# Kernel optimization log

Measured on AMD Instinct MI355X. Metric: run time of the kernel, lower is better.

Reference implementation:

```python
import jax, jax.numpy as jnp
import numpy as np

LMAX = 4
S2_DIM = (LMAX + 1) ** 2                                  # 25: s2 irreps, mul 1 per l
SO3_DIM = sum((2 * l + 1) ** 2 for l in range(LMAX + 1))  # 165: so3 irreps, mul 2l+1 per l
B = 2048
F_S2, F_SO3 = 1, 16
N_S2_KERNEL = 48      # s2_healpix_grid(rec_level=1)
N_SO3_KERNEL = 192    # so3_near_identity_grid()
N_ACT_GRID = 4000     # SO3Activation resolution=10, aspect_ratio=2 -> 20x10x20, flattened
N_EVAL = 4608         # so3_healpix_grid(rec_level=2): 192 pixels x 24 gamma


def setup_inputs() -> dict:
    ks = jax.random.split(jax.random.key(0), 7)
    return {
        "x": jax.random.normal(ks[0], (B, F_S2, S2_DIM), jnp.float32),
        "w_s2": jax.random.normal(ks[1], (F_S2, F_SO3, N_S2_KERNEL), jnp.float32),
        "Y": jax.random.normal(ks[2], (N_S2_KERNEL, S2_DIM), jnp.float32),
        "w_so3": jax.random.normal(ks[3], (F_SO3, 1, N_SO3_KERNEL), jnp.float32),
        "D_kernel": jax.random.normal(ks[4], (N_SO3_KERNEL, SO3_DIM), jnp.float32),
        "D_act": jax.random.normal(ks[5], (N_ACT_GRID, SO3_DIM), jnp.float32),
        "eval_wigners": jax.random.normal(ks[6], (SO3_DIM, N_EVAL), jnp.float32) / np.sqrt(SO3_DIM),
    }


def _s2_to_so3_linear(x, psi):
    # e3nn o3.Linear(s2_irreps -> so3_irreps, f_in, f_out, external weights)
    # x:   [B, f_in, 25]  (mul 1 per degree l)
    # psi: [f_in, f_out, 25] ; column l^2+j is the weight to output-multiplicity j of degree l
    f_in, f_out = psi.shape[0], psi.shape[1]
    out, s = [], 0
    for l in range(LMAX + 1):
        d = 2 * l + 1
        x_l = x[..., s:s + d]                       # [B, f_in, d]
        p_l = psi[..., s:s + d]                     # [f_in, f_out, d] (j = out-mul idx)
        o = jnp.einsum('bxm,xyj->byjm', x_l, p_l) / np.sqrt(f_in)
        out.append(o.reshape(x.shape[0], f_out, d * d))
        s += d
    return jnp.concatenate(out, axis=-1)            # [B, f_out, 165]


def _so3_to_so3_linear(x, psi):
    # e3nn o3.Linear(so3_irreps -> so3_irreps, f_in, f_out, external weights)
    # x:   [B, f_in, 165] ; psi: [f_in, f_out, 165]
    f_in, f_out = psi.shape[0], psi.shape[1]
    out, s = [], 0
    for l in range(LMAX + 1):
        d = 2 * l + 1
        x_l = x[..., s:s + d * d].reshape(x.shape[0], f_in, d, d)   # [B,f_in,u,m]
        p_l = psi[..., s:s + d * d].reshape(f_in, f_out, d, d)      # [f_in,f_out,u,v]
        o = jnp.einsum('bxum,xyuv->byvm', x_l, p_l) / np.sqrt(f_in * d)
        out.append(o.reshape(x.shape[0], f_out, d * d))
        s += d * d
    return jnp.concatenate(out, axis=-1)            # [B, f_out, 165]


def _forward(x, w_s2, Y, w_so3, D_kernel, D_act, eval_wigners):
    # --- S2Convolution: kernel = SH-transform of grid weights, then irrep-wise linear
    psi1 = jnp.einsum('ni,xyn->xyi', Y, w_s2) / np.sqrt(N_S2_KERNEL)     # [1,16,25]
    h = _s2_to_so3_linear(x, psi1)                                        # [B,16,165]
    # --- SO3Activation: Fourier -> SO(3) grid -> relu -> Fourier
    g = jnp.einsum('bfi,gi->bfg', h, D_act) / np.sqrt(SO3_DIM)            # [B,16,4000]
    g = jax.nn.relu(g)
    h = jnp.einsum('bfg,gi->bfi', g, D_act) * (np.sqrt(SO3_DIM) / N_ACT_GRID)
    # --- SO3Convolution
    psi2 = jnp.einsum('ni,xyn->xyi', D_kernel, w_so3) / np.sqrt(N_SO3_KERNEL)  # [16,1,165]
    harmonics = _so3_to_so3_linear(h, psi2)                               # [B,1,165]
    # --- compute_probabilities: matmul with eval Wigner-D basis + softmax over grid
    probs = jax.nn.softmax(jnp.einsum('bfi,ie->be', harmonics, eval_wigners), axis=1)  # [B,4608]
    # --- top-k masking: zero out everything below the 5th-highest prob of sample 0
    fifth = jax.lax.top_k(probs, 5)[0][0, 4]
    probs = jnp.where(probs < fifth, 0.0, probs)
    return harmonics, probs


def reference(x, w_s2, Y, w_so3, D_kernel, D_act, eval_wigners):
    return _forward(x, w_s2, Y, w_so3, D_kernel, D_act, eval_wigners)
```

## Files before the change

### kernel.cpp

```cpp
#include <hip/hip_runtime.h>

typedef short bf16x8 __attribute__((ext_vector_type(8)));
typedef float f32x16 __attribute__((ext_vector_type(16)));
typedef int   i32x4  __attribute__((ext_vector_type(4)));

#define INV_SQRT165 0.07784989441615349f
#define FINAL_SCALE 0.0032113081446662823f
#define ZERO16 ((f32x16){0.f,0.f,0.f,0.f,0.f,0.f,0.f,0.f,0.f,0.f,0.f,0.f,0.f,0.f,0.f,0.f})

__device__ __forceinline__ unsigned short f2bf(float f) {
  unsigned int u = __builtin_bit_cast(unsigned int, f);
  unsigned int r = (u + 0x7FFFu + ((u >> 16) & 1u)) >> 16;
  return (unsigned short)r;
}
__device__ __forceinline__ float bf2f(unsigned short h) {
  unsigned int u = ((unsigned int)h) << 16;
  return __builtin_bit_cast(float, u);
}
__device__ __forceinline__ unsigned int pack_bf2f(float lo, float hi) {
  unsigned int a = (__builtin_bit_cast(unsigned int, lo) + 0x8000u) >> 16;
  unsigned int b = (__builtin_bit_cast(unsigned int, hi) + 0x8000u) & 0xFFFF0000u;
  return b | a;
}

__device__ __forceinline__ void gl_lds16(const void* g, void* l) {
  __builtin_amdgcn_global_load_lds(
      (const __attribute__((address_space(1))) unsigned int*)(unsigned long long)g,
      (__attribute__((address_space(3))) unsigned int*)(unsigned int)(unsigned long long)l,
      16, 0, 0);
}

__device__ __forceinline__ void decode_i(int i, int& lv, int& rel) {
  if (i < 1)       { lv = 0; rel = i; }
  else if (i < 10) { lv = 1; rel = i - 1; }
  else if (i < 35) { lv = 2; rel = i - 10; }
  else if (i < 84) { lv = 3; rel = i - 35; }
  else             { lv = 4; rel = i - 84; }
}
__device__ __forceinline__ int divq(int rel, int lv) {
  const int mag[5] = {32768, 10923, 6554, 4682, 3641};
  return (rel * mag[lv]) >> 15;
}

__device__ __forceinline__ int gperm(int p) {
  int a = p & 3, hlp = (p >> 2) & 1, c = p >> 3;
  return ((c >> 1) << 4) + hlp * 8 + ((c & 1) << 2) + a;
}

__global__ __launch_bounds__(256) void prep_k(const float* __restrict__ Da,
                                              const float* __restrict__ ew,
                                              const float* __restrict__ Y,
                                              const float* __restrict__ w_s2,
                                              const float* __restrict__ Dk,
                                              const float* __restrict__ w_so3,
                                              unsigned short* __restrict__ e1pre,
                                              unsigned short* __restrict__ d2pre,
                                              unsigned short* __restrict__ ewpre,
                                              float* __restrict__ psi2) {
  __shared__ __align__(16) unsigned short lds[13824];
  const int tid = threadIdx.x;
  const int l = tid & 63, hl = l >> 5, ln = l & 31;
  if (blockIdx.x < 128) {
    const int ci = blockIdx.x, g0 = ci * 32;
    float* psi1L = (float*)(lds + 6464);
    for (int e = tid; e < 6400; e += 256) lds[e] = 0;
    for (int e = tid; e < 400; e += 256) {
      int yv = e / 25, iv = e % 25;
      float s = 0.f;
      for (int n = 0; n < 48; n++) s += Y[n * 25 + iv] * w_s2[yv * 48 + n];
      psi1L[e] = s * 0.14433756729740643f;
    }
    __syncthreads();
    int rows = 4000 - g0; if (rows > 32) rows = 32; if (rows < 0) rows = 0;
    int ne = rows * 165;
    for (int e = tid; e < ne; e += 256) {
      int gl_ = e / 165, k = e - gl_ * 165;
      lds[gl_ * 200 + k] = f2bf(Da[g0 * 165 + e]);
    }
    __syncthreads();
#pragma unroll
    for (int it = 0; it < 3; it++) {
      int tt = it * 4 + (tid >> 6);
      int nf = tt >> 1, gk = tt & 1;
      unsigned short v[8];
#pragma unroll
      for (int j = 0; j < 8; j++)
        v[j] = lds[(gk * 16 + hl * 8 + j) * 200 + nf * 32 + ln];
      *(i32x4*)(d2pre + ci * 6144 + tt * 512 + l * 8) = *(i32x4*)v;
    }
    for (int yy = 0; yy < 16; yy++) {
#pragma unroll
      for (int it = 0; it < 4; it++) {
        int idx = it * 256 + tid;
        int kf = idx >> 9, r2 = idx & 511;
        int ll = r2 >> 3, j = r2 & 7;
        int lnn = ll & 31, hll = ll >> 5;
        int k = kf * 16 + hll * 8 + j;
        unsigned short ov = 0;
        if (k < 25) {
          int lv = (k < 1) ? 0 : (k < 4) ? 1 : (k < 9) ? 2 : (k < 16) ? 3 : 4;
          int d = 2 * lv + 1;
          int m = k - lv * lv;
          int off165 = lv * (4 * lv * lv - 1) / 3;
          int gp = gperm(lnn);
          float s = 0.f;
          const float* pr = psi1L + yy * 25 + lv * lv;
          const unsigned short* dr = lds + gp * 200 + off165 + m;
          for (int j2 = 0; j2 < d; j2++) s += pr[j2] * bf2f(dr[j2 * d]);
          ov = f2bf(s * INV_SQRT165);
        }
        e1pre[((yy * 128 + ci) * 2 + kf) * 512 + ll * 8 + j] = ov;
      }
    }
  } else if (blockIdx.x < 200) {
    const int bx2 = blockIdx.x - 128;
    const int n0 = bx2 * 64;
    for (int e = tid; e < 13824; e += 256) lds[e] = 0;
    __syncthreads();
    for (int e = tid; e < 10560; e += 256) {
      int k = e >> 6, n = e & 63;
      lds[k * 72 + n] = f2bf(ew[k * 4608 + n0 + n]);
    }
    __syncthreads();
#pragma unroll
    for (int it = 0; it < 6; it++) {
      int tb = it * 4 + (tid >> 6);
      int nt2 = tb / 12, kf = tb - nt2 * 12;
      unsigned short v[8];
#pragma unroll
      for (int j = 0; j < 8; j++)
        v[j] = lds[(kf * 16 + hl * 8 + j) * 72 + nt2 * 32 + ln];
      *(i32x4*)(ewpre + (bx2 * 2 + nt2) * 6144 + kf * 512 + l * 8) = *(i32x4*)v;
    }
  } else {
    int t = (blockIdx.x - 200) * 256 + tid;
    if (t < 2640) {
      int ch = t / 165, i = t % 165;
      float s = 0.f;
      for (int n = 0; n < 192; n++) s += Dk[n * 165 + i] * w_so3[ch * 192 + n];
      psi2[t] = s * (0.07216878364870323f * FINAL_SCALE);
    }
  }
}

__global__ __launch_bounds__(256, 2) void fused_mlp_k(
    const float* __restrict__ x,
    const unsigned short* __restrict__ e1pre,
    const unsigned short* __restrict__ d2pre,
    unsigned short* __restrict__ part)
{
  __shared__ __align__(16) unsigned char smem[57344];
  const int tid = threadIdx.x;
  const int w = tid >> 6, l = tid & 63;
  const int hl = l >> 5, ln = l & 31;
  const int h = blockIdx.x & 1;
  const int y = (blockIdx.x >> 1) & 15;
  const int btg = blockIdx.x >> 5;
  const int bw = w >> 1, ng = w & 1;
  const int c0 = h * 64;

  bf16x8 xf[2][2];
#pragma unroll
  for (int t = 0; t < 2; t++) {
    const float* xr = x + (btg * 128 + bw * 64 + t * 32 + ln) * 25;
#pragma unroll
    for (int kf = 0; kf < 2; kf++) {
      unsigned short v[8];
#pragma unroll
      for (int j = 0; j < 8; j++) {
        int k = kf * 16 + hl * 8 + j;
        v[j] = (k < 25) ? f2bf(xr[k]) : (unsigned short)0;
      }
      xf[t][kf] = *(bf16x8*)v;
    }
  }

  f32x16 o[6];
#pragma unroll
  for (int i = 0; i < 6; i++) o[i] = ZERO16;

  const unsigned short* ebase = e1pre + (y * 128) * 1024;

#pragma unroll
  for (int i = 0; i < 7; i++) {
    int tb = w * 7 + i;
    int cc = (tb >= 14), tb2 = tb - cc * 14;
    const unsigned short* g = (tb2 < 12)
        ? (d2pre + (c0 + cc) * 6144 + tb2 * 512 + l * 8)
        : (ebase + ((c0 + cc) * 2 + (tb2 - 12)) * 512 + l * 8);
    gl_lds16(g, smem + cc * 14336 + tb2 * 1024);
  }

  for (int it = 0; it < 32; it++) {
    __syncthreads();
    const unsigned char* buf = smem + (it & 1) * 28672;
    if (it < 31) {
      unsigned char* nb = smem + ((it + 1) & 1) * 28672;
      const int c = c0 + (it + 1) * 2;
#pragma unroll
      for (int i = 0; i < 7; i++) {
        int tb = w * 7 + i;
        int cc = (tb >= 14), tb2 = tb - cc * 14;
        const unsigned short* g = (tb2 < 12)
            ? (d2pre + (c + cc) * 6144 + tb2 * 512 + l * 8)
            : (ebase + ((c + cc) * 2 + (tb2 - 12)) * 512 + l * 8);
        gl_lds16(g, nb + cc * 14336 + tb2 * 1024);
      }
    }

#pragma unroll
    for (int cc = 0; cc < 2; cc++) {
      const unsigned char* cb = buf + cc * 14336;
      bf16x8 aE0 = *(const bf16x8*)(cb + 12288 + l * 16);
      bf16x8 aE1 = *(const bf16x8*)(cb + 13312 + l * 16);
      f32x16 s0 = ZERO16, s1 = ZERO16;
      s0 = __builtin_amdgcn_mfma_f32_32x32x16_bf16(aE0, xf[0][0], s0, 0, 0, 0);
      s1 = __builtin_amdgcn_mfma_f32_32x32x16_bf16(aE0, xf[1][0], s1, 0, 0, 0);
      s0 = __builtin_amdgcn_mfma_f32_32x32x16_bf16(aE1, xf[0][1], s0, 0, 0, 0);
      s1 = __builtin_amdgcn_mfma_f32_32x32x16_bf16(aE1, xf[1][1], s1, 0, 0, 0);

      bf16x8 a2[2][2];
#pragma unroll
      for (int t = 0; t < 2; t++) {
        const f32x16& sv = t ? s1 : s0;
        unsigned int dw[8];
#pragma unroll
        for (int p = 0; p < 8; p++)
          dw[p] = pack_bf2f(fmaxf(sv[2 * p], 0.f), fmaxf(sv[2 * p + 1], 0.f));
        i32x4 q0 = (i32x4){(int)dw[0], (int)dw[1], (int)dw[2], (int)dw[3]};
        i32x4 q1 = (i32x4){(int)dw[4], (int)dw[5], (int)dw[6], (int)dw[7]};
        a2[t][0] = __builtin_bit_cast(bf16x8, q0);
        a2[t][1] = __builtin_bit_cast(bf16x8, q1);
      }

#pragma unroll
      for (int gk = 0; gk < 2; gk++) {
#pragma unroll
        for (int nf = 0; nf < 3; nf++) {
          bf16x8 b2 = *(const bf16x8*)(cb + ((ng * 3 + nf) * 2 + gk) * 1024 + l * 16);
          o[nf]     = __builtin_amdgcn_mfma_f32_32x32x16_bf16(a2[0][gk], b2, o[nf],     0, 0, 0);
          o[3 + nf] = __builtin_amdgcn_mfma_f32_32x32x16_bf16(a2[1][gk], b2, o[3 + nf], 0, 0, 0);
        }
      }
    }
  }

#pragma unroll
  for (int t = 0; t < 2; t++) {
    unsigned short* pp = part + (size_t)((h * 16 + y) * 2048 + btg * 128 + bw * 64 + t * 32) * 192;
#pragma unroll
    for (int nf = 0; nf < 3; nf++) {
      int n = ng * 96 + nf * 32 + ln;
      if (n < 176) {
#pragma unroll
        for (int r = 0; r < 16; r++) {
          int row = (r & 3) + 8 * (r >> 2) + 4 * hl;
          pp[row * 192 + n] = f2bf(o[t * 3 + nf][r]);
        }
      }
    }
  }
}

__global__ __launch_bounds__(256) void so3_k(const unsigned short* __restrict__ part,
                                             const float* __restrict__ psi2,
                                             float* __restrict__ harm_out,
                                             unsigned short* __restrict__ harmbpre) {
  __shared__ float lds[4 * 16 * 180];
  __shared__ float p2s[2640];
  const int tid = threadIdx.x;
  const int b0 = blockIdx.x * 4;
  for (int e = tid; e < 2640; e += 256) p2s[e] = psi2[e];
  {
    const int ybl = tid >> 2;
    const int yy = ybl & 15, bloc = ybl >> 4;
    const int s = tid & 3;
    const unsigned int* r0 = (const unsigned int*)(part + ((size_t)(0 * 16 + yy) * 2048 + b0 + bloc) * 192);
    const unsigned int* r1 = (const unsigned int*)(part + ((size_t)(1 * 16 + yy) * 2048 + b0 + bloc) * 192);
    float* dst = lds + (bloc * 16 + yy) * 180;
#pragma unroll
    for (int t = 0; t < 22; t++) {
      int d = s * 22 + t;
      if (d < 88) {
        unsigned int u0 = r0[d], u1 = r1[d];
        int n0 = d * 2;
        dst[n0]     = bf2f((unsigned short)(u0 & 0xFFFF)) + bf2f((unsigned short)(u1 & 0xFFFF));
        dst[n0 + 1] = bf2f((unsigned short)(u0 >> 16))    + bf2f((unsigned short)(u1 >> 16));
      }
    }
  }
  __syncthreads();
  for (int jj = tid; jj < 768; jj += 256) {
    int e = (jj * 683) >> 17;
    int i = jj - e * 192;
    int bb = b0 + e;
    unsigned short* hb = harmbpre + (((bb >> 5) * 12 + (i >> 4)) << 9)
                       + ((i >> 3) & 1) * 256 + (bb & 31) * 8 + (i & 7);
    if (i < 165) {
      const float* row0 = lds + e * (16 * 180);
      int lv, rel; decode_i(i, lv, rel);
      int d = 2 * lv + 1;
      int off = i - rel;
      int v = divq(rel, lv), m = rel - v * d;
      float s = 0.f;
      for (int ch = 0; ch < 16; ch++) {
        const float* rw = row0 + ch * 180 + off;
        const float* p2 = p2s + ch * 165 + off;
        for (int u = 0; u < d; u++) s += rw[u * d + m] * p2[u * d + v];
      }
      s *= 0.25f * rsqrtf((float)d);
      harm_out[bb * 165 + i] = s;
      *hb = f2bf(s);
    } else {
      *hb = 0;
    }
  }
}

__global__ __launch_bounds__(64) void eval_k(
    const unsigned short* __restrict__ harmbpre,
    const unsigned short* __restrict__ ewpre,
    float* __restrict__ logits,
    float* __restrict__ logit0)
{
  const int l = threadIdx.x;
  const int hl = l >> 5, ln = l & 31;
  const int mt = blockIdx.y;
  const int n0 = blockIdx.x * 192;

  bf16x8 a[12];
  const short* ap = (const short*)harmbpre + mt * 6144 + l * 8;
#pragma unroll
  for (int kf = 0; kf < 12; kf++) a[kf] = *(const bf16x8*)(ap + kf * 512);

  f32x16 acc[6];
#pragma unroll
  for (int nf = 0; nf < 6; nf++) acc[nf] = ZERO16;

  const short* bp = (const short*)ewpre + (blockIdx.x * 6) * 6144 + l * 8;
#pragma unroll
  for (int kf = 0; kf < 12; kf++) {
#pragma unroll
    for (int nf = 0; nf < 6; nf++) {
      bf16x8 b = *(const bf16x8*)(bp + nf * 6144 + kf * 512);
      acc[nf] = __builtin_amdgcn_mfma_f32_32x32x16_bf16(a[kf], b, acc[nf], 0, 0, 0);
    }
  }
#pragma unroll
  for (int nf = 0; nf < 6; nf++) {
    const int col = n0 + nf * 32 + ln;
#pragma unroll
    for (int r = 0; r < 16; r++) {
      int row = (r & 3) + 8 * (r >> 2) + 4 * hl;
      logits[(mt * 32 + row) * 4608 + col] = acc[nf][r];
    }
  }
  if (mt == 0 && hl == 0) {
#pragma unroll
    for (int nf = 0; nf < 6; nf++) logit0[n0 + nf * 32 + ln] = acc[nf][0];
  }
}

__global__ __launch_bounds__(256) void smthresh_k(float* __restrict__ probs,
                                                  const float* __restrict__ logit0) {
  __shared__ float buf[4608];
  __shared__ float sm[8], ss[8];
  __shared__ float wv[4]; __shared__ int wi[4];
  __shared__ float gbest;
  float* p = probs + (size_t)blockIdx.x * 4608;
  const int tid = threadIdx.x;
  const int l = tid & 63, w = tid >> 6;
  float v[18];
  float mx = -3.4e38f, mx0 = -3.4e38f;
#pragma unroll
  for (int i = 0; i < 18; i++) {
    v[i] = p[i * 256 + tid];
    float t0 = logit0[i * 256 + tid];
    buf[i * 256 + tid] = t0;
    mx = fmaxf(mx, v[i]);
    mx0 = fmaxf(mx0, t0);
  }
#pragma unroll
  for (int off = 32; off >= 1; off >>= 1) {
    mx = fmaxf(mx, __shfl_xor(mx, off));
    mx0 = fmaxf(mx0, __shfl_xor(mx0, off));
  }
  if (l == 0) { sm[w] = mx; sm[4 + w] = mx0; }
  __syncthreads();
  mx  = fmaxf(fmaxf(sm[0], sm[1]), fmaxf(sm[2], sm[3]));
  mx0 = fmaxf(fmaxf(sm[4], sm[5]), fmaxf(sm[6], sm[7]));
  float s = 0.f, s0 = 0.f;
#pragma unroll
  for (int i = 0; i < 18; i++) {
    v[i] = __expf(v[i] - mx); s += v[i];
    s0 += __expf(buf[i * 256 + tid] - mx0);
  }
#pragma unroll
  for (int off = 32; off >= 1; off >>= 1) { s += __shfl_xor(s, off); s0 += __shfl_xor(s0, off); }
  if (l == 0) { ss[w] = s; ss[4 + w] = s0; }
  __syncthreads();
  s  = ss[0] + ss[1] + ss[2] + ss[3];
  s0 = ss[4] + ss[5] + ss[6] + ss[7];
  float inv = 1.f / s, inv0 = 1.f / s0;

  float ff = 0.f;
  for (int it = 0; it < 5; it++) {
    float bm = -3.4e38f; int bi = 0;
    for (int i = tid; i < 4608; i += 256) {
      float xx = buf[i];
      if (xx > bm) { bm = xx; bi = i; }
    }
    for (int off = 32; off >= 1; off >>= 1) {
      float ov = __shfl_xor(bm, off); int oi = __shfl_xor(bi, off);
      if (ov > bm) { bm = ov; bi = oi; }
    }
    if (l == 0) { wv[w] = bm; wi[w] = bi; }
    __syncthreads();
    if (tid == 0) {
      float B = wv[0]; int I = wi[0];
      for (int k = 1; k < 4; k++) if (wv[k] > B) { B = wv[k]; I = wi[k]; }
      gbest = B;
      buf[I] = -3.4e38f;
    }
    __syncthreads();
    ff = gbest;
    __syncthreads();
  }
  float t = __expf(ff - mx0) * inv0;
#pragma unroll
  for (int i = 0; i < 18; i++) {
    float pv = v[i] * inv;
    p[i * 256 + tid] = (pv < t) ? 0.f : pv;
  }
}

extern "C" void kernel_launch(void* const* d_in, const int* in_sizes, int n_in,
                              void* d_out, int out_size, void* d_ws, size_t ws_size,
                              hipStream_t stream) {
  const float* x     = (const float*)d_in[0];
  const float* w_s2  = (const float*)d_in[1];
  const float* Y     = (const float*)d_in[2];
  const float* w_so3 = (const float*)d_in[3];
  const float* Dk    = (const float*)d_in[4];
  const float* Da    = (const float*)d_in[5];
  const float* ew    = (const float*)d_in[6];

  float* out = (float*)d_out;
  float* harm_out = out;
  float* probs    = out + 337920;
  unsigned short* part = (unsigned short*)probs;

  char* ws = (char*)d_ws;
  float* psi2  = (float*)(ws + 0);
  unsigned short* e1pre    = (unsigned short*)(ws + 12288);
  unsigned short* d2pre    = (unsigned short*)(ws + 4206592);
  unsigned short* ewpre    = (unsigned short*)(ws + 5779456);
  unsigned short* harmbpre = (unsigned short*)(ws + 7548928);
  float* logit0 = (float*)(ws + 8335360);

  prep_k<<<211, 256, 0, stream>>>(Da, ew, Y, w_s2, Dk, w_so3, e1pre, d2pre, ewpre, psi2);
  fused_mlp_k<<<512, 256, 0, stream>>>(x, e1pre, d2pre, part);
  so3_k<<<512, 256, 0, stream>>>(part, psi2, harm_out, harmbpre);
  eval_k<<<dim3(24, 64), 64, 0, stream>>>(harmbpre, ewpre, probs, logit0);
  smthresh_k<<<2048, 256, 0, stream>>>(probs, logit0);
}
```

Measured before the change: 245.0 us.

## Split fused MLP reduction three ways and retile warps to whole N per batch tile

The fused MLP kernel now splits the 125-chunk grid reduction into three partial sums instead of two, launching 768 blocks. Each warp now owns 32 batch rows and all six N fragments instead of 64 rows and three fragments. Shared memory per block is halved by staging one chunk per iteration, and the launch bound asks for three blocks per CU. The intent is more parallelism and occupancy. In exchange, the x-side first GEMM is repeated less efficiently, each block does more iterations with less work each, and so3_k reads and adds a third partial buffer.

```diff
diff --git a/kernel.cpp b/kernel.cpp
--- a/kernel.cpp
+++ b/kernel.cpp
@@ -143,26 +143,26 @@
   }
 }
 
-__global__ __launch_bounds__(256, 2) void fused_mlp_k(
+__global__ __launch_bounds__(256, 3) void fused_mlp_k(
     const float* __restrict__ x,
     const unsigned short* __restrict__ e1pre,
     const unsigned short* __restrict__ d2pre,
     unsigned short* __restrict__ part)
 {
-  __shared__ __align__(16) unsigned char smem[57344];
+  __shared__ __align__(16) unsigned char smem[28672];
   const int tid = threadIdx.x;
   const int w = tid >> 6, l = tid & 63;
   const int hl = l >> 5, ln = l & 31;
-  const int h = blockIdx.x & 1;
-  const int y = (blockIdx.x >> 1) & 15;
-  const int btg = blockIdx.x >> 5;
-  const int bw = w >> 1, ng = w & 1;
-  const int c0 = h * 64;
-
-  bf16x8 xf[2][2];
-#pragma unroll
-  for (int t = 0; t < 2; t++) {
-    const float* xr = x + (btg * 128 + bw * 64 + t * 32 + ln) * 25;
+  const int h = blockIdx.x >> 8;
+  const int y = (blockIdx.x >> 4) & 15;
+  const int btg = blockIdx.x & 15;
+  const int bt = btg * 4 + w;
+  const int c0 = (h == 0) ? 0 : (h == 1) ? 43 : 86;
+  const int cnt = (h == 2) ? 42 : 43;
+
+  bf16x8 xf[2];
+  {
+    const float* xr = x + (bt * 32 + ln) * 25;
 #pragma unroll
     for (int kf = 0; kf < 2; kf++) {
       unsigned short v[8];
@@ -171,7 +171,7 @@
         int k = kf * 16 + hl * 8 + j;
         v[j] = (k < 25) ? f2bf(xr[k]) : (unsigned short)0;
       }
-      xf[t][kf] = *(bf16x8*)v;
+      xf[kf] = *(bf16x8*)v;
     }
   }
 
@@ -182,81 +182,64 @@
   const unsigned short* ebase = e1pre + (y * 128) * 1024;
 
 #pragma unroll
-  for (int i = 0; i < 7; i++) {
-    int tb = w * 7 + i;
-    int cc = (tb >= 14), tb2 = tb - cc * 14;
-    const unsigned short* g = (tb2 < 12)
-        ? (d2pre + (c0 + cc) * 6144 + tb2 * 512 + l * 8)
-        : (ebase + ((c0 + cc) * 2 + (tb2 - 12)) * 512 + l * 8);
-    gl_lds16(g, smem + cc * 14336 + tb2 * 1024);
-  }
-
-  for (int it = 0; it < 32; it++) {
-    __syncthreads();
-    const unsigned char* buf = smem + (it & 1) * 28672;
-    if (it < 31) {
-      unsigned char* nb = smem + ((it + 1) & 1) * 28672;
-      const int c = c0 + (it + 1) * 2;
-#pragma unroll
-      for (int i = 0; i < 7; i++) {
-        int tb = w * 7 + i;
-        int cc = (tb >= 14), tb2 = tb - cc * 14;
-        const unsigned short* g = (tb2 < 12)
-            ? (d2pre + (c + cc) * 6144 + tb2 * 512 + l * 8)
-            : (ebase + ((c + cc) * 2 + (tb2 - 12)) * 512 + l * 8);
-        gl_lds16(g, nb + cc * 14336 + tb2 * 1024);
-      }
-    }
-
-#pragma unroll
-    for (int cc = 0; cc < 2; cc++) {
-      const unsigned char* cb = buf + cc * 14336;
-      bf16x8 aE0 = *(const bf16x8*)(cb + 12288 + l * 16);
-      bf16x8 aE1 = *(const bf16x8*)(cb + 13312 + l * 16);
-      f32x16 s0 = ZERO16, s1 = ZERO16;
-      s0 = __builtin_amdgcn_mfma_f32_32x32x16_bf16(aE0, xf[0][0], s0, 0, 0, 0);
-      s1 = __builtin_amdgcn_mfma_f32_32x32x16_bf16(aE0, xf[1][0], s1, 0, 0, 0);
-      s0 = __builtin_amdgcn_mfma_f32_32x32x16_bf16(aE1, xf[0][1], s0, 0, 0, 0);
-      s1 = __builtin_amdgcn_mfma_f32_32x32x16_bf16(aE1, xf[1][1], s1, 0, 0, 0);
-
-      bf16x8 a2[2][2];
-#pragma unroll
-      for (int t = 0; t < 2; t++) {
-        const f32x16& sv = t ? s1 : s0;
-        unsigned int dw[8];
-#pragma unroll
-        for (int p = 0; p < 8; p++)
-          dw[p] = pack_bf2f(fmaxf(sv[2 * p], 0.f), fmaxf(sv[2 * p + 1], 0.f));
-        i32x4 q0 = (i32x4){(int)dw[0], (int)dw[1], (int)dw[2], (int)dw[3]};
-        i32x4 q1 = (i32x4){(int)dw[4], (int)dw[5], (int)dw[6], (int)dw[7]};
-        a2[t][0] = __builtin_bit_cast(bf16x8, q0);
-        a2[t][1] = __builtin_bit_cast(bf16x8, q1);
-      }
-
-#pragma unroll
-      for (int gk = 0; gk < 2; gk++) {
-#pragma unroll
-        for (int nf = 0; nf < 3; nf++) {
-          bf16x8 b2 = *(const bf16x8*)(cb + ((ng * 3 + nf) * 2 + gk) * 1024 + l * 16);
-          o[nf]     = __builtin_amdgcn_mfma_f32_32x32x16_bf16(a2[0][gk], b2, o[nf],     0, 0, 0);
-          o[3 + nf] = __builtin_amdgcn_mfma_f32_32x32x16_bf16(a2[1][gk], b2, o[3 + nf], 0, 0, 0);
+  for (int i = 0; i < 4; i++) {
+    int tb = w * 4 + i;
+    if (tb < 14) {
+      const unsigned short* g = (tb < 12) ? (d2pre + c0 * 6144 + tb * 512 + l * 8)
+                                          : (ebase + (c0 * 2 + (tb - 12)) * 512 + l * 8);
+      gl_lds16(g, smem + tb * 1024);
+    }
+  }
+
+  for (int ci = 0; ci < cnt; ci++) {
+    __syncthreads();
+    const unsigned char* cb = smem + (ci & 1) * 14336;
+    if (ci + 1 < cnt) {
+      unsigned char* nb = smem + ((ci + 1) & 1) * 14336;
+      const int c = c0 + ci + 1;
+#pragma unroll
+      for (int i = 0; i < 4; i++) {
+        int tb = w * 4 + i;
+        if (tb < 14) {
+          const unsigned short* g = (tb < 12) ? (d2pre + c * 6144 + tb * 512 + l * 8)
+                                              : (ebase + (c * 2 + (tb - 12)) * 512 + l * 8);
+          gl_lds16(g, nb + tb * 1024);
         }
       }
     }
-  }
-
-#pragma unroll
-  for (int t = 0; t < 2; t++) {
-    unsigned short* pp = part + (size_t)((h * 16 + y) * 2048 + btg * 128 + bw * 64 + t * 32) * 192;
-#pragma unroll
-    for (int nf = 0; nf < 3; nf++) {
-      int n = ng * 96 + nf * 32 + ln;
-      if (n < 176) {
-#pragma unroll
-        for (int r = 0; r < 16; r++) {
-          int row = (r & 3) + 8 * (r >> 2) + 4 * hl;
-          pp[row * 192 + n] = f2bf(o[t * 3 + nf][r]);
-        }
+    bf16x8 aE0 = *(const bf16x8*)(cb + 12288 + l * 16);
+    bf16x8 aE1 = *(const bf16x8*)(cb + 13312 + l * 16);
+    f32x16 s = ZERO16;
+    s = __builtin_amdgcn_mfma_f32_32x32x16_bf16(aE0, xf[0], s, 0, 0, 0);
+    s = __builtin_amdgcn_mfma_f32_32x32x16_bf16(aE1, xf[1], s, 0, 0, 0);
+    unsigned int dw[8];
+#pragma unroll
+    for (int p = 0; p < 8; p++)
+      dw[p] = pack_bf2f(fmaxf(s[2 * p], 0.f), fmaxf(s[2 * p + 1], 0.f));
+    i32x4 q0 = (i32x4){(int)dw[0], (int)dw[1], (int)dw[2], (int)dw[3]};
+    i32x4 q1 = (i32x4){(int)dw[4], (int)dw[5], (int)dw[6], (int)dw[7]};
+    bf16x8 a20 = __builtin_bit_cast(bf16x8, q0);
+    bf16x8 a21 = __builtin_bit_cast(bf16x8, q1);
+#pragma unroll
+    for (int gk = 0; gk < 2; gk++) {
+      bf16x8 a2 = gk ? a21 : a20;
+#pragma unroll
+      for (int nf = 0; nf < 6; nf++) {
+        bf16x8 b2 = *(const bf16x8*)(cb + (nf * 2 + gk) * 1024 + l * 16);
+        o[nf] = __builtin_amdgcn_mfma_f32_32x32x16_bf16(a2, b2, o[nf], 0, 0, 0);
+      }
+    }
+  }
+
+  unsigned short* pp = part + (size_t)((h * 16 + y) * 2048 + bt * 32) * 192;
+#pragma unroll
+  for (int nf = 0; nf < 6; nf++) {
+    int n = nf * 32 + ln;
+    if (n < 176) {
+#pragma unroll
+      for (int r = 0; r < 16; r++) {
+        int row = (r & 3) + 8 * (r >> 2) + 4 * hl;
+        pp[row * 192 + n] = f2bf(o[nf][r]);
       }
     }
   }
@@ -277,15 +260,18 @@
     const int s = tid & 3;
     const unsigned int* r0 = (const unsigned int*)(part + ((size_t)(0 * 16 + yy) * 2048 + b0 + bloc) * 192);
     const unsigned int* r1 = (const unsigned int*)(part + ((size_t)(1 * 16 + yy) * 2048 + b0 + bloc) * 192);
+    const unsigned int* r2 = (const unsigned int*)(part + ((size_t)(2 * 16 + yy) * 2048 + b0 + bloc) * 192);
     float* dst = lds + (bloc * 16 + yy) * 180;
 #pragma unroll
     for (int t = 0; t < 22; t++) {
       int d = s * 22 + t;
       if (d < 88) {
-        unsigned int u0 = r0[d], u1 = r1[d];
+        unsigned int u0 = r0[d], u1 = r1[d], u2 = r2[d];
         int n0 = d * 2;
-        dst[n0]     = bf2f((unsigned short)(u0 & 0xFFFF)) + bf2f((unsigned short)(u1 & 0xFFFF));
-        dst[n0 + 1] = bf2f((unsigned short)(u0 >> 16))    + bf2f((unsigned short)(u1 >> 16));
+        dst[n0]     = bf2f((unsigned short)(u0 & 0xFFFF)) + bf2f((unsigned short)(u1 & 0xFFFF))
+                    + bf2f((unsigned short)(u2 & 0xFFFF));
+        dst[n0 + 1] = bf2f((unsigned short)(u0 >> 16)) + bf2f((unsigned short)(u1 >> 16))
+                    + bf2f((unsigned short)(u2 >> 16));
       }
     }
   }
@@ -459,7 +445,7 @@
   float* logit0 = (float*)(ws + 8335360);
 
   prep_k<<<211, 256, 0, stream>>>(Da, ew, Y, w_s2, Dk, w_so3, e1pre, d2pre, ewpre, psi2);
-  fused_mlp_k<<<512, 256, 0, stream>>>(x, e1pre, d2pre, part);
+  fused_mlp_k<<<768, 256, 0, stream>>>(x, e1pre, d2pre, part);
   so3_k<<<512, 256, 0, stream>>>(part, psi2, harm_out, harmbpre);
   eval_k<<<dim3(24, 64), 64, 0, stream>>>(harmbpre, ewpre, probs, logit0);
   smthresh_k<<<2048, 256, 0, stream>>>(probs, logit0);
```

Measured after the change: 235.3 us. -3.9%, faster.
